# Performance work log

Measured on AMD Instinct MI355X. Metric: run time of the kernel, lower is better.

## Reference

```python
import jax, jax.numpy as jnp
import numpy as np

DIM = 128
HID = 128
EPS = 1e-5

def setup_inputs() -> dict:
    key = jax.random.key(0)
    ks = jax.random.split(key, 9)
    s = 1.0 / np.sqrt(DIM)
    sh = 1.0 / np.sqrt(HID)
    return {
        "pair_repr": jax.random.normal(ks[0], (1, 512, 512, DIM), dtype=jnp.float32),
        "Wl": jax.random.uniform(ks[1], (DIM, HID), jnp.float32, -s, s),
        "bl": jax.random.uniform(ks[2], (HID,), jnp.float32, -s, s),
        "Wr": jax.random.uniform(ks[3], (DIM, HID), jnp.float32, -s, s),
        "br": jax.random.uniform(ks[4], (HID,), jnp.float32, -s, s),
        "Wo": jax.random.uniform(ks[5], (HID, DIM), jnp.float32, -sh, sh),
        "bo": jax.random.uniform(ks[6], (DIM,), jnp.float32, -sh, sh),
        "Wg": jax.random.uniform(ks[7], (DIM, DIM), jnp.float32, -s, s),
        "bg": jax.random.uniform(ks[8], (DIM,), jnp.float32, -s, s),
        "gamma": jnp.ones((DIM,), jnp.float32),
        "beta": jnp.zeros((DIM,), jnp.float32),
    }

def reference(pair_repr, Wl, bl, Wr, br, Wo, bo, Wg, bg, gamma, beta):
    # left/right projections: (B, L, L, H)
    left = pair_repr @ Wl + bl
    right = pair_repr @ Wr + br
    # triangle multiplication: out[b,i,j,h] = sum_k left[b,i,k,h] * right[b,k,j,h]
    out = jnp.einsum('bikh,bkjh->bijh', left, right)
    out = out @ Wo + bo
    gate = jax.nn.sigmoid(pair_repr @ Wg + bg)
    out = pair_repr + gate * out
    # LayerNorm over last dim
    mu = jnp.mean(out, axis=-1, keepdims=True)
    var = jnp.mean((out - mu) ** 2, axis=-1, keepdims=True)
    return (out - mu) * jax.lax.rsqrt(var + EPS) * gamma + beta
```

## Files before the change

kernel.cpp:

```cpp
#include <hip/hip_runtime.h>
#include <hip/hip_bf16.h>


#define LSZ 512
#define NPOS (LSZ * LSZ)

typedef short s16;
typedef __attribute__((ext_vector_type(4))) short s16x4;
typedef __attribute__((ext_vector_type(8))) short s16x8;
typedef __attribute__((ext_vector_type(4))) float f32x4;

typedef const __attribute__((address_space(1))) unsigned int* gas1;
typedef __attribute__((address_space(3))) unsigned int* las3;

static __device__ __forceinline__ s16 f2bf(float f) {
    unsigned int u = __builtin_bit_cast(unsigned int, f);
    u += 0x7FFFu + ((u >> 16) & 1u);
    return (s16)(u >> 16);
}

static __device__ __forceinline__ unsigned pkbf(float x, float y) {
    __hip_bfloat162 h = __float22bfloat162_rn(make_float2(x, y));
    unsigned u;
    __builtin_memcpy(&u, &h, 4);
    return u;
}
static __device__ __forceinline__ s16x8 cvt8(f32x4 a, f32x4 b) {
    union { s16x8 v; unsigned u[4]; } r;
    r.u[0] = pkbf(a[0], a[1]);
    r.u[1] = pkbf(a[2], a[3]);
    r.u[2] = pkbf(b[0], b[1]);
    r.u[3] = pkbf(b[2], b[3]);
    return r.v;
}
static __device__ __forceinline__ s16x4 cvt4(float x0, float x1, float x2, float x3) {
    union { s16x4 v; unsigned u[2]; } r;
    r.u[0] = pkbf(x0, x1);
    r.u[1] = pkbf(x2, x3);
    return r.v;
}

static __device__ __forceinline__ void gload_lds16(const void* g, void* l) {
    __builtin_amdgcn_global_load_lds((gas1)g, (las3)l, 16, 0, 0);
}

#define WAITVM(N) asm volatile("s_waitcnt vmcnt(" #N ")" ::: "memory")

__global__ void k_prep(const float* __restrict__ Wl, const float* __restrict__ Wr,
                       const float* __restrict__ Wg, const float* __restrict__ Wo,
                       s16* __restrict__ WlT, s16* __restrict__ WrT,
                       s16* __restrict__ WgT, s16* __restrict__ WoT) {
    const float* src;
    s16* dst;
    switch (blockIdx.x) {
        case 0: src = Wl; dst = WlT; break;
        case 1: src = Wr; dst = WrT; break;
        case 2: src = Wg; dst = WgT; break;
        default: src = Wo; dst = WoT; break;
    }
    for (int e = threadIdx.x; e < 128 * 128; e += blockDim.x) {
        int o = e >> 7, i = e & 127;
        dst[e] = f2bf(src[i * 128 + o]);
    }
}

#define PSUB(BUF, SUB, META) do {                                                     \
    const int row_ = (SUB) * 16 + lr;                                                 \
    const char* pbp_ = (const char*)&PA[BUF][0] + row_ * 512;                         \
    f32x4 acc_ = (f32x4){0.f, 0.f, 0.f, 0.f};                                         \
    _Pragma("unroll")                                                                 \
    for (int ks = 0; ks < 4; ++ks) {                                                  \
        f32x4 pa0_ = *(const f32x4*)(pbp_ + ((((ks << 3) | (lg << 1)) ^ rsw) << 4));  \
        f32x4 pa1_ = *(const f32x4*)(pbp_ + (((((ks << 3) | (lg << 1)) + 1) ^ rsw) << 4)); \
        s16x8 pf_ = cvt8(pa0_, pa1_);                                                 \
        acc_ = __builtin_amdgcn_mfma_f32_16x16x32_bf16(wv[ks], pf_, acc_, 0, 0, 0);   \
    }                                                                                 \
    const long pbase_ = COLMODE ? ((long)((META) >> 4) * 512 + (((META) & 15) << 5) + row_) \
                                : ((long)(META) * 32 + row_);                         \
    _Pragma("unroll")                                                                 \
    for (int r = 0; r < 4; ++r)                                                       \
        outT[(long)(dl + r) * NPOS + pbase_] = f2bf(acc_[r] + b4[r]);                 \
} while (0)

#define PITER(M, NLIT, DOPF) do {                                                     \
    WAITVM(NLIT);                                                                     \
    __builtin_amdgcn_s_barrier();                                                     \
    PSUB((M) & 1, 0, meta0 + (M));                                                    \
    PSUB((M) & 1, 1, meta0 + (M));                                                    \
    asm volatile("s_waitcnt lgkmcnt(0)" ::: "memory");                                \
    __builtin_amdgcn_s_barrier();                                                     \
    __builtin_amdgcn_sched_barrier(0);                                                \
    if (DOPF) stage((M) & 1, meta0 + (M) + 2);                                        \
} while (0)

template <int COLMODE>
__global__ __launch_bounds__(512, 4) void k_proj(const float* __restrict__ pair,
                                                 const s16* __restrict__ WT,
                                                 const float* __restrict__ bias,
                                                 s16* __restrict__ outT) {
    __shared__ __align__(16) float PA[2][32 * 128];
    const int t = threadIdx.x;
    const int w = t >> 6, l = t & 63;
    const int lr = l & 15, lg = l >> 4;
    const int d0 = w << 4;
    const int dl = d0 + (lg << 2);
    const int rsw = lr & 7;
    s16x8 wv[4];
#pragma unroll
    for (int ks = 0; ks < 4; ++ks)
        wv[ks] = *(const s16x8*)(WT + (d0 + lr) * 128 + ks * 32 + lg * 8);
    const f32x4 b4 = *(const f32x4*)(bias + dl);
    const long meta0 = (long)blockIdx.x * 8;

    auto stage = [&](int buf, long meta) {
        {
            const int row = t >> 5, u = t & 31;
            const long gp = COLMODE ? (((meta & 15) * 32 + row) * 512 + (meta >> 4))
                                    : (meta * 32 + row);
            gload_lds16(pair + gp * 128 + ((u ^ (row & 7)) << 2),
                        (char*)&PA[buf][0] + t * 16);
        }
        {
            const int row = 16 + (t >> 5), u = t & 31;
            const long gp = COLMODE ? (((meta & 15) * 32 + row) * 512 + (meta >> 4))
                                    : (meta * 32 + row);
            gload_lds16(pair + gp * 128 + ((u ^ (row & 7)) << 2),
                        (char*)&PA[buf][0] + 8192 + t * 16);
        }
    };

    stage(0, meta0 + 0);
    stage(1, meta0 + 1);
    PITER(0, 2, 1);
    PITER(1, 2, 1);
    PITER(2, 2, 1);
    PITER(3, 2, 1);
    PITER(4, 2, 1);
    PITER(5, 2, 1);
    PITER(6, 2, 0);
    PITER(7, 0, 0);
}

__global__ __launch_bounds__(512, 1) void k_tri(const s16* __restrict__ leftT,
                                                const s16* __restrict__ rightTT,
                                                s16* __restrict__ tri) {
    __shared__ __align__(16) s16 As[2][256 * 64];
    __shared__ __align__(16) s16 Bs[2][256 * 64];
    const int t = threadIdx.x;
    const int logical = ((blockIdx.x & 7) << 6) | (blockIdx.x >> 3);
    const int h = logical >> 2;
    const int ti = (logical >> 1) & 1, tj = logical & 1;
    const s16* Ap = leftT + (long)h * NPOS + (long)ti * 256 * 512;
    const s16* Bp = rightTT + (long)h * NPOS + (long)tj * 256 * 512;
    const int w = t >> 6, l = t & 63;
    const int wr = (w >> 2) * 128, wc = (w & 3) * 64;
    const int lr = l & 15, lg = l >> 4;

    auto stage = [&](int buf, int kb) {
#pragma unroll
        for (int P = 0; P < 4; ++P) {
            const int unit = P * 512 + t;
            const int row = unit >> 3, u = unit & 7;
            const int kks = (u ^ (row & 7)) << 3;
            gload_lds16(Ap + (long)row * 512 + kb + kks, (char*)&As[buf][0] + unit * 16);
            gload_lds16(Bp + (long)row * 512 + kb + kks, (char*)&Bs[buf][0] + unit * 16);
        }
    };

    f32x4 acc[8][4];
#pragma unroll
    for (int mi = 0; mi < 8; ++mi)
#pragma unroll
        for (int ni = 0; ni < 4; ++ni) acc[mi][ni] = (f32x4){0.f, 0.f, 0.f, 0.f};

    stage(0, 0);
    stage(1, 64);
#pragma unroll
    for (int k = 0; k < 8; ++k) {
        if (k < 7) { WAITVM(8); } else { WAITVM(0); }
        __builtin_amdgcn_s_barrier();
        const int buf = k & 1;
#pragma unroll
        for (int ks = 0; ks < 2; ++ks) {
            s16x8 af[8], bfv[4];
#pragma unroll
            for (int mi = 0; mi < 8; ++mi) {
                const int row = wr + mi * 16 + lr;
                af[mi] = *(const s16x8*)((const char*)&As[buf][0] + row * 128 + (((ks * 4 + lg) ^ (row & 7)) << 4));
            }
#pragma unroll
            for (int ni = 0; ni < 4; ++ni) {
                const int row = wc + ni * 16 + lr;
                bfv[ni] = *(const s16x8*)((const char*)&Bs[buf][0] + row * 128 + (((ks * 4 + lg) ^ (row & 7)) << 4));
            }
#pragma unroll
            for (int mi = 0; mi < 8; ++mi)
#pragma unroll
                for (int ni = 0; ni < 4; ++ni)
                    acc[mi][ni] = __builtin_amdgcn_mfma_f32_16x16x32_bf16(af[mi], bfv[ni], acc[mi][ni], 0, 0, 0);
        }
        asm volatile("s_waitcnt lgkmcnt(0)" ::: "memory");
        __builtin_amdgcn_s_barrier();
        __builtin_amdgcn_sched_barrier(0);
        if (k + 2 < 8) stage(buf, (k + 2) * 64);
    }
#pragma unroll
    for (int mi = 0; mi < 8; ++mi) {
#pragma unroll
        for (int r = 0; r < 4; ++r) {
            const int i = ti * 256 + wr + mi * 16 + lg * 4 + r;
            s16* dst = tri + (long)h * NPOS + (long)i * 512 + tj * 256 + wc;
#pragma unroll
            for (int ni = 0; ni < 4; ++ni) dst[ni * 16 + lr] = f2bf(acc[mi][ni][r]);
        }
    }
}

#define SUBTILE(BUF, SUB) do {                                                        \
    const int row_ = (SUB) * 16 + lr;                                                 \
    const int po_ = row_ >> 3, p3_ = row_ & 7;                                        \
    const char* pbp_ = (const char*)&PA[BUF][0] + row_ * 512;                         \
    f32x4 accO_ = (f32x4){0.f, 0.f, 0.f, 0.f};                                        \
    f32x4 accG_ = (f32x4){0.f, 0.f, 0.f, 0.f};                                        \
    _Pragma("unroll")                                                                 \
    for (int ks = 0; ks < 4; ++ks) {                                                  \
        const int kk = ks * 32 + lg * 8;                                              \
        s16x8 tbv_;                                                                   \
        _Pragma("unroll")                                                             \
        for (int j = 0; j < 8; ++j) {                                                 \
            const int hh_ = kk + j;                                                   \
            tbv_[j] = TRI[BUF][(hh_ * 4 + (po_ ^ ((hh_ >> 3) & 3))) * 8 + p3_];       \
        }                                                                             \
        f32x4 pa0_ = *(const f32x4*)(pbp_ + ((((ks << 3) | (lg << 1)) ^ rsw) << 4));  \
        f32x4 pa1_ = *(const f32x4*)(pbp_ + (((((ks << 3) | (lg << 1)) + 1) ^ rsw) << 4)); \
        s16x8 pf_ = cvt8(pa0_, pa1_);                                                 \
        accO_ = __builtin_amdgcn_mfma_f32_16x16x32_bf16(wo[ks], tbv_, accO_, 0, 0, 0);\
        accG_ = __builtin_amdgcn_mfma_f32_16x16x32_bf16(wg[ks], pf_, accG_, 0, 0, 0); \
    }                                                                                 \
    f32x4 rs_ = *(const f32x4*)(pbp_ + ((((w << 2) | lg) ^ rsw) << 4));               \
    f32x4 xr_;                                                                        \
    _Pragma("unroll")                                                                 \
    for (int r = 0; r < 4; ++r) {                                                     \
        const float gate_ = 1.f / (1.f + __expf(-(accG_[r] + bg4[r])));               \
        xr_[r] = rs_[r] + gate_ * (accO_[r] + bo4[r]);                                \
    }                                                                                 \
    *(f32x4*)&xbuf[row_][dl] = xr_;                                                   \
} while (0)

#define LNPASS(P, META) do {                                                          \
    const int row_ = (P) * 16 + (t >> 5);                                             \
    f32x4 xv_ = *(const f32x4*)&xbuf[row_][lnc];                                      \
    float s_ = xv_[0] + xv_[1] + xv_[2] + xv_[3];                                     \
    s_ += __shfl_xor(s_, 1); s_ += __shfl_xor(s_, 2); s_ += __shfl_xor(s_, 4);        \
    s_ += __shfl_xor(s_, 8); s_ += __shfl_xor(s_, 16);                                \
    const float mu_ = s_ * 0.0078125f;                                                \
    float v_ = 0.f;                                                                   \
    _Pragma("unroll")                                                                 \
    for (int j = 0; j < 4; ++j) { float dd_ = xv_[j] - mu_; v_ += dd_ * dd_; }        \
    v_ += __shfl_xor(v_, 1); v_ += __shfl_xor(v_, 2); v_ += __shfl_xor(v_, 4);        \
    v_ += __shfl_xor(v_, 8); v_ += __shfl_xor(v_, 16);                                \
    const float rstd_ = rsqrtf(v_ * 0.0078125f + 1e-5f);                              \
    f32x4 o_;                                                                         \
    _Pragma("unroll")                                                                 \
    for (int j = 0; j < 4; ++j) o_[j] = (xv_[j] - mu_) * rstd_ * gm4[j] + bt4[j];     \
    *(f32x4*)(out + ((META) * 32 + row_) * 128 + lnc) = o_;                           \
} while (0)

#define ITER(M, NLIT, DOPF) do {                                                      \
    WAITVM(NLIT);                                                                     \
    __builtin_amdgcn_s_barrier();                                                     \
    SUBTILE((M) & 1, 0);                                                              \
    SUBTILE((M) & 1, 1);                                                              \
    asm volatile("s_waitcnt lgkmcnt(0)" ::: "memory");                                \
    __builtin_amdgcn_s_barrier();                                                     \
    __builtin_amdgcn_sched_barrier(0);                                                \
    if (DOPF) stage((M) & 1, meta0 + (M) + 2);                                        \
    LNPASS(0, meta0 + (M));                                                           \
    LNPASS(1, meta0 + (M));                                                           \
} while (0)

__global__ __launch_bounds__(512, 2) void k_final(const float* __restrict__ pair,
                                                  const s16* __restrict__ tri,
                                                  const s16* __restrict__ WgT,
                                                  const s16* __restrict__ WoT,
                                                  const float* __restrict__ bgv,
                                                  const float* __restrict__ bov,
                                                  const float* __restrict__ gam,
                                                  const float* __restrict__ bet,
                                                  float* __restrict__ out) {
    __shared__ __align__(16) s16 TRI[2][32 * 128];
    __shared__ __align__(16) float PA[2][32 * 128];
    __shared__ __align__(16) float xbuf[32][132];
    const int t = threadIdx.x;
    const int w = t >> 6, l = t & 63;
    const int lr = l & 15, lg = l >> 4;
    const int d0 = w << 4;
    const int dl = d0 + (lg << 2);
    const int rsw = lr & 7;
    s16x8 wo[4], wg[4];
#pragma unroll
    for (int ks = 0; ks < 4; ++ks) {
        wo[ks] = *(const s16x8*)(WoT + (d0 + lr) * 128 + ks * 32 + lg * 8);
        wg[ks] = *(const s16x8*)(WgT + (d0 + lr) * 128 + ks * 32 + lg * 8);
    }
    const f32x4 bo4 = *(const f32x4*)(bov + dl);
    const f32x4 bg4 = *(const f32x4*)(bgv + dl);
    const int lnc = (t & 31) << 2;
    const f32x4 gm4 = *(const f32x4*)(gam + lnc);
    const f32x4 bt4 = *(const f32x4*)(bet + lnc);
    const long meta0 = (long)blockIdx.x * 8;

    auto stage = [&](int buf, long meta) {
        const long pb = meta * 32;
        {
            const int hh = t >> 2;
            const int po = (t & 3) ^ ((hh >> 3) & 3);
            gload_lds16(tri + (long)hh * NPOS + pb + po * 8,
                        (char*)&TRI[buf][0] + t * 16);
        }
        {
            const int row = t >> 5, u = t & 31;
            gload_lds16(pair + (pb + row) * 128 + ((u ^ (row & 7)) << 2),
                        (char*)&PA[buf][0] + t * 16);
        }
        {
            const int row = 16 + (t >> 5), u = t & 31;
            gload_lds16(pair + (pb + row) * 128 + ((u ^ (row & 7)) << 2),
                        (char*)&PA[buf][0] + 8192 + t * 16);
        }
    };

    stage(0, meta0 + 0);
    stage(1, meta0 + 1);
    ITER(0, 3, 1);
    ITER(1, 3, 1);
    ITER(2, 3, 1);
    ITER(3, 3, 1);
    ITER(4, 3, 1);
    ITER(5, 3, 1);
    ITER(6, 3, 0);
    ITER(7, 0, 0);
}

extern "C" void kernel_launch(void* const* d_in, const int* in_sizes, int n_in,
                              void* d_out, int out_size, void* d_ws, size_t ws_size,
                              hipStream_t stream) {
    const float* pair = (const float*)d_in[0];
    const float* Wl   = (const float*)d_in[1];
    const float* bl   = (const float*)d_in[2];
    const float* Wr   = (const float*)d_in[3];
    const float* br   = (const float*)d_in[4];
    const float* Wo   = (const float*)d_in[5];
    const float* bo   = (const float*)d_in[6];
    const float* Wg   = (const float*)d_in[7];
    const float* bg   = (const float*)d_in[8];
    const float* gam  = (const float*)d_in[9];
    const float* bet  = (const float*)d_in[10];
    float* out = (float*)d_out;

    s16* WlT = (s16*)d_ws;
    s16* WrT = WlT + 128 * 128;
    s16* WgT = WrT + 128 * 128;
    s16* WoT = WgT + 128 * 128;
    s16* leftT   = WoT + 128 * 128;
    s16* rightTT = leftT + (long)128 * NPOS;
    s16* tri     = rightTT + (long)128 * NPOS;

    k_prep<<<4, 256, 0, stream>>>(Wl, Wr, Wg, Wo, WlT, WrT, WgT, WoT);
    k_proj<0><<<1024, 512, 0, stream>>>(pair, WlT, bl, leftT);
    k_proj<1><<<1024, 512, 0, stream>>>(pair, WrT, br, rightTT);
    k_tri<<<512, 512, 0, stream>>>(leftT, rightTT, tri);
    k_final<<<1024, 512, 0, stream>>>(pair, tri, WgT, WoT, bg, bo, gam, bet, out);
}
```

Baseline: 243.9 us.

## Shrink k_final blocks to 256 threads with 16-row tiles and two output column groups per wave

```diff
diff --git a/kernel.cpp b/kernel.cpp
--- a/kernel.cpp
+++ b/kernel.cpp
@@ -31,12 +31,6 @@
     r.u[1] = pkbf(a[2], a[3]);
     r.u[2] = pkbf(b[0], b[1]);
     r.u[3] = pkbf(b[2], b[3]);
-    return r.v;
-}
-static __device__ __forceinline__ s16x4 cvt4(float x0, float x1, float x2, float x3) {
-    union { s16x4 v; unsigned u[2]; } r;
-    r.u[0] = pkbf(x0, x1);
-    r.u[1] = pkbf(x2, x3);
     return r.v;
 }
 
@@ -216,12 +210,15 @@
     }
 }
 
-#define SUBTILE(BUF, SUB) do {                                                        \
-    const int row_ = (SUB) * 16 + lr;                                                 \
-    const int po_ = row_ >> 3, p3_ = row_ & 7;                                        \
+#define XST 132
+#define SUBTILE(BUF) do {                                                             \
+    const int row_ = lr;                                                              \
+    const int po_ = lr >> 3, p3_ = lr & 7;                                            \
     const char* pbp_ = (const char*)&PA[BUF][0] + row_ * 512;                         \
-    f32x4 accO_ = (f32x4){0.f, 0.f, 0.f, 0.f};                                        \
-    f32x4 accG_ = (f32x4){0.f, 0.f, 0.f, 0.f};                                        \
+    f32x4 accO0_ = (f32x4){0.f, 0.f, 0.f, 0.f};                                       \
+    f32x4 accO1_ = (f32x4){0.f, 0.f, 0.f, 0.f};                                       \
+    f32x4 accG0_ = (f32x4){0.f, 0.f, 0.f, 0.f};                                       \
+    f32x4 accG1_ = (f32x4){0.f, 0.f, 0.f, 0.f};                                       \
     _Pragma("unroll")                                                                 \
     for (int ks = 0; ks < 4; ++ks) {                                                  \
         const int kk = ks * 32 + lg * 8;                                              \
@@ -229,57 +226,74 @@
         _Pragma("unroll")                                                             \
         for (int j = 0; j < 8; ++j) {                                                 \
             const int hh_ = kk + j;                                                   \
-            tbv_[j] = TRI[BUF][(hh_ * 4 + (po_ ^ ((hh_ >> 3) & 3))) * 8 + p3_];       \
+            tbv_[j] = TRI[BUF][(hh_ * 2 + (po_ ^ ((hh_ >> 3) & 1))) * 8 + p3_];       \
         }                                                                             \
         f32x4 pa0_ = *(const f32x4*)(pbp_ + ((((ks << 3) | (lg << 1)) ^ rsw) << 4));  \
         f32x4 pa1_ = *(const f32x4*)(pbp_ + (((((ks << 3) | (lg << 1)) + 1) ^ rsw) << 4)); \
         s16x8 pf_ = cvt8(pa0_, pa1_);                                                 \
-        accO_ = __builtin_amdgcn_mfma_f32_16x16x32_bf16(wo[ks], tbv_, accO_, 0, 0, 0);\
-        accG_ = __builtin_amdgcn_mfma_f32_16x16x32_bf16(wg[ks], pf_, accG_, 0, 0, 0); \
-    }                                                                                 \
-    f32x4 rs_ = *(const f32x4*)(pbp_ + ((((w << 2) | lg) ^ rsw) << 4));               \
-    f32x4 xr_;                                                                        \
+        accO0_ = __builtin_amdgcn_mfma_f32_16x16x32_bf16(wo0[ks], tbv_, accO0_, 0, 0, 0); \
+        accO1_ = __builtin_amdgcn_mfma_f32_16x16x32_bf16(wo1[ks], tbv_, accO1_, 0, 0, 0); \
+        accG0_ = __builtin_amdgcn_mfma_f32_16x16x32_bf16(wg0[ks], pf_, accG0_, 0, 0, 0);  \
+        accG1_ = __builtin_amdgcn_mfma_f32_16x16x32_bf16(wg1[ks], pf_, accG1_, 0, 0, 0);  \
+    }                                                                                 \
+    f32x4 rs0_ = *(const f32x4*)(pbp_ + ((((w << 3) | lg) ^ rsw) << 4));              \
+    f32x4 rs1_ = *(const f32x4*)(pbp_ + ((((w << 3) | 4 | lg) ^ rsw) << 4));          \
+    f32x4 x0_, x1_;                                                                   \
     _Pragma("unroll")                                                                 \
     for (int r = 0; r < 4; ++r) {                                                     \
-        const float gate_ = 1.f / (1.f + __expf(-(accG_[r] + bg4[r])));               \
-        xr_[r] = rs_[r] + gate_ * (accO_[r] + bo4[r]);                                \
-    }                                                                                 \
-    *(f32x4*)&xbuf[row_][dl] = xr_;                                                   \
-} while (0)
-
-#define LNPASS(P, META) do {                                                          \
-    const int row_ = (P) * 16 + (t >> 5);                                             \
-    f32x4 xv_ = *(const f32x4*)&xbuf[row_][lnc];                                      \
-    float s_ = xv_[0] + xv_[1] + xv_[2] + xv_[3];                                     \
-    s_ += __shfl_xor(s_, 1); s_ += __shfl_xor(s_, 2); s_ += __shfl_xor(s_, 4);        \
-    s_ += __shfl_xor(s_, 8); s_ += __shfl_xor(s_, 16);                                \
+        const float g0_ = 1.f / (1.f + __expf(-(accG0_[r] + bg40[r])));               \
+        x0_[r] = rs0_[r] + g0_ * (accO0_[r] + bo40[r]);                               \
+        const float g1_ = 1.f / (1.f + __expf(-(accG1_[r] + bg41[r])));               \
+        x1_[r] = rs1_[r] + g1_ * (accO1_[r] + bo41[r]);                               \
+    }                                                                                 \
+    *(f32x4*)&xbuf[row_ * XST + dl] = x0_;                                            \
+    *(f32x4*)&xbuf[row_ * XST + dl + 16] = x1_;                                       \
+} while (0)
+
+#define LNPASS(META) do {                                                             \
+    const int row_ = t >> 4;                                                          \
+    f32x4 xa_ = *(const f32x4*)&xbuf[row_ * XST + lnc];                               \
+    f32x4 xb_ = *(const f32x4*)&xbuf[row_ * XST + lnc + 4];                           \
+    float s_ = xa_[0] + xa_[1] + xa_[2] + xa_[3] + xb_[0] + xb_[1] + xb_[2] + xb_[3]; \
+    s_ += __shfl_xor(s_, 1); s_ += __shfl_xor(s_, 2);                                 \
+    s_ += __shfl_xor(s_, 4); s_ += __shfl_xor(s_, 8);                                 \
     const float mu_ = s_ * 0.0078125f;                                                \
     float v_ = 0.f;                                                                   \
     _Pragma("unroll")                                                                 \
-    for (int j = 0; j < 4; ++j) { float dd_ = xv_[j] - mu_; v_ += dd_ * dd_; }        \
-    v_ += __shfl_xor(v_, 1); v_ += __shfl_xor(v_, 2); v_ += __shfl_xor(v_, 4);        \
-    v_ += __shfl_xor(v_, 8); v_ += __shfl_xor(v_, 16);                                \
+    for (int j = 0; j < 4; ++j) {                                                     \
+        float da_ = xa_[j] - mu_; v_ += da_ * da_;                                    \
+        float db_ = xb_[j] - mu_; v_ += db_ * db_;                                    \
+    }                                                                                 \
+    v_ += __shfl_xor(v_, 1); v_ += __shfl_xor(v_, 2);                                 \
+    v_ += __shfl_xor(v_, 4); v_ += __shfl_xor(v_, 8);                                 \
     const float rstd_ = rsqrtf(v_ * 0.0078125f + 1e-5f);                              \
-    f32x4 o_;                                                                         \
-    _Pragma("unroll")                                                                 \
-    for (int j = 0; j < 4; ++j) o_[j] = (xv_[j] - mu_) * rstd_ * gm4[j] + bt4[j];     \
-    *(f32x4*)(out + ((META) * 32 + row_) * 128 + lnc) = o_;                           \
+    f32x4 ga_ = *(const f32x4*)(gam + lnc);                                           \
+    f32x4 gb_ = *(const f32x4*)(gam + lnc + 4);                                       \
+    f32x4 ba_ = *(const f32x4*)(bet + lnc);                                           \
+    f32x4 bb_ = *(const f32x4*)(bet + lnc + 4);                                       \
+    f32x4 oa_, ob_;                                                                   \
+    _Pragma("unroll")                                                                 \
+    for (int j = 0; j < 4; ++j) {                                                     \
+        oa_[j] = (xa_[j] - mu_) * rstd_ * ga_[j] + ba_[j];                            \
+        ob_[j] = (xb_[j] - mu_) * rstd_ * gb_[j] + bb_[j];                            \
+    }                                                                                 \
+    float* op_ = out + ((META) * 16 + row_) * 128 + lnc;                              \
+    __builtin_nontemporal_store(oa_, (f32x4*)op_);                                    \
+    __builtin_nontemporal_store(ob_, (f32x4*)(op_ + 4));                              \
 } while (0)
 
 #define ITER(M, NLIT, DOPF) do {                                                      \
     WAITVM(NLIT);                                                                     \
     __builtin_amdgcn_s_barrier();                                                     \
-    SUBTILE((M) & 1, 0);                                                              \
-    SUBTILE((M) & 1, 1);                                                              \
+    SUBTILE((M) & 1);                                                                 \
     asm volatile("s_waitcnt lgkmcnt(0)" ::: "memory");                                \
     __builtin_amdgcn_s_barrier();                                                     \
     __builtin_amdgcn_sched_barrier(0);                                                \
     if (DOPF) stage((M) & 1, meta0 + (M) + 2);                                        \
-    LNPASS(0, meta0 + (M));                                                           \
-    LNPASS(1, meta0 + (M));                                                           \
-} while (0)
-
-__global__ __launch_bounds__(512, 2) void k_final(const float* __restrict__ pair,
+    LNPASS(meta0 + (M));                                                              \
+} while (0)
+
+__global__ __launch_bounds__(256, 4) void k_final(const float* __restrict__ pair,
                                                   const s16* __restrict__ tri,
                                                   const s16* __restrict__ WgT,
                                                   const s16* __restrict__ WoT,
@@ -288,33 +302,35 @@
                                                   const float* __restrict__ gam,
                                                   const float* __restrict__ bet,
                                                   float* __restrict__ out) {
-    __shared__ __align__(16) s16 TRI[2][32 * 128];
-    __shared__ __align__(16) float PA[2][32 * 128];
-    __shared__ __align__(16) float xbuf[32][132];
+    __shared__ __align__(16) s16 TRI[2][16 * 128];
+    __shared__ __align__(16) float PA[2][16 * 128];
+    __shared__ __align__(16) float xbuf[16 * XST];
     const int t = threadIdx.x;
     const int w = t >> 6, l = t & 63;
     const int lr = l & 15, lg = l >> 4;
-    const int d0 = w << 4;
+    const int d0 = w << 5;
     const int dl = d0 + (lg << 2);
     const int rsw = lr & 7;
-    s16x8 wo[4], wg[4];
+    s16x8 wo0[4], wo1[4], wg0[4], wg1[4];
 #pragma unroll
     for (int ks = 0; ks < 4; ++ks) {
-        wo[ks] = *(const s16x8*)(WoT + (d0 + lr) * 128 + ks * 32 + lg * 8);
-        wg[ks] = *(const s16x8*)(WgT + (d0 + lr) * 128 + ks * 32 + lg * 8);
-    }
-    const f32x4 bo4 = *(const f32x4*)(bov + dl);
-    const f32x4 bg4 = *(const f32x4*)(bgv + dl);
-    const int lnc = (t & 31) << 2;
-    const f32x4 gm4 = *(const f32x4*)(gam + lnc);
-    const f32x4 bt4 = *(const f32x4*)(bet + lnc);
+        wo0[ks] = *(const s16x8*)(WoT + (d0 + lr) * 128 + ks * 32 + lg * 8);
+        wo1[ks] = *(const s16x8*)(WoT + (d0 + 16 + lr) * 128 + ks * 32 + lg * 8);
+        wg0[ks] = *(const s16x8*)(WgT + (d0 + lr) * 128 + ks * 32 + lg * 8);
+        wg1[ks] = *(const s16x8*)(WgT + (d0 + 16 + lr) * 128 + ks * 32 + lg * 8);
+    }
+    const f32x4 bo40 = *(const f32x4*)(bov + dl);
+    const f32x4 bo41 = *(const f32x4*)(bov + dl + 16);
+    const f32x4 bg40 = *(const f32x4*)(bgv + dl);
+    const f32x4 bg41 = *(const f32x4*)(bgv + dl + 16);
+    const int lnc = (t & 15) << 3;
     const long meta0 = (long)blockIdx.x * 8;
 
     auto stage = [&](int buf, long meta) {
-        const long pb = meta * 32;
-        {
-            const int hh = t >> 2;
-            const int po = (t & 3) ^ ((hh >> 3) & 3);
+        const long pb = meta * 16;
+        {
+            const int hh = t >> 1;
+            const int po = (t & 1) ^ ((hh >> 3) & 1);
             gload_lds16(tri + (long)hh * NPOS + pb + po * 8,
                         (char*)&TRI[buf][0] + t * 16);
         }
@@ -324,9 +340,9 @@
                         (char*)&PA[buf][0] + t * 16);
         }
         {
-            const int row = 16 + (t >> 5), u = t & 31;
+            const int row = 8 + (t >> 5), u = t & 31;
             gload_lds16(pair + (pb + row) * 128 + ((u ^ (row & 7)) << 2),
-                        (char*)&PA[buf][0] + 8192 + t * 16);
+                        (char*)&PA[buf][0] + 4096 + t * 16);
         }
     };
 
@@ -370,5 +386,5 @@
     k_proj<0><<<1024, 512, 0, stream>>>(pair, WlT, bl, leftT);
     k_proj<1><<<1024, 512, 0, stream>>>(pair, WrT, br, rightTT);
     k_tri<<<512, 512, 0, stream>>>(leftT, rightTT, tri);
-    k_final<<<1024, 512, 0, stream>>>(pair, tri, WgT, WoT, bg, bo, gam, bet, out);
-}
+    k_final<<<2048, 256, 0, stream>>>(pair, tri, WgT, WoT, bg, bo, gam, bet, out);
+}
```

Measured after the change: 382.0 us. 56.6% more time.
